# Kernel tuning notes

Measured on AMD Instinct MI355X. Metric: run time of the kernel, lower is better.

The kernel has to match this reference:

```python
import jax, jax.numpy as jnp
import numpy as np

E = 32      # particle_embed_dim = q/k/v head out dim
G = 2       # nof_net_types (conv groups)
NEG_SLOPE = 0.01


def _glin(x, w, b, groups):
    """Grouped 1x1 conv on (M, C, 1, 1) == grouped linear.
    x: (M, Cin), w: (Cout, Cin//groups), b: (Cout,)."""
    M = x.shape[0]
    Cout = w.shape[0]
    xg = x.reshape(M, groups, -1)                 # (M, G, Cin/G)
    wg = w.reshape(groups, Cout // groups, -1)    # (G, Cout/G, Cin/G)
    y = jnp.einsum('mgi,goi->mgo', xg, wg).reshape(M, Cout)
    return y + b


def setup_inputs() -> dict:
    key = jax.random.key(0)
    ks = jax.random.split(key, 9)
    B, N = 32, 1024
    s = 0.05
    return {
        'x_e':   jax.random.normal(ks[0], (B, N, G * E), dtype=jnp.float32),
        'w_qkv': jax.random.normal(ks[1], (3 * G * E, E), dtype=jnp.float32) * s,
        'b_qkv': jax.random.normal(ks[2], (3 * G * E,), dtype=jnp.float32) * s,
        'w_h1':  jax.random.normal(ks[3], (G * E, 2 * E), dtype=jnp.float32) * s,
        'b_h1':  jax.random.normal(ks[4], (G * E,), dtype=jnp.float32) * s,
        'w_h10': jax.random.normal(ks[5], (G * E, E), dtype=jnp.float32) * s,
        'b_h10': jax.random.normal(ks[6], (G * E,), dtype=jnp.float32) * s,
        'w_h11': jax.random.normal(ks[7], (G * E, E), dtype=jnp.float32) * s,
        'b_h11': jax.random.normal(ks[8], (G * E,), dtype=jnp.float32) * s,
    }


def reference(x_e, w_qkv, b_qkv, w_h1, b_h1, w_h10, b_h10, w_h11, b_h11):
    B, N, D = x_e.shape                      # D = G*E = 64
    act = lambda z: jnp.where(z >= 0, z, NEG_SLOPE * z)

    # grouped 1x1-conv QKV projection
    qkv = _glin(x_e.reshape(B * N, D), w_qkv, b_qkv, G)        # (B*N, 3*G*E)
    qkv = qkv.reshape(B, N, G, 3, E).transpose(0, 2, 3, 1, 4)  # (B, G, 3, N, E)
    q, k, v = qkv[:, :, 0], qkv[:, :, 1], qkv[:, :, 2]         # each (B, G, N, E)

    # NOTE: module divides k by sqrt(E) and logits by sqrt(E) again -> 1/E total
    scale = 1.0 / E
    ip = jnp.einsum('bgne,bgme->bgnm', q, k) * scale           # (B, G, N, N)
    sip = jax.nn.softmax(ip, axis=-1)
    attn = jnp.einsum('bgnm,bgme->bgne', sip, v)               # (B, G, N, E)

    # concat pre-attention v with attention output, regroup per-particle
    x_xe = jnp.concatenate([v, attn], axis=3)                  # (B, G, N, 2E)
    x_xe = x_xe.transpose(0, 2, 1, 3).reshape(B * N, G * 2 * E)  # (B*N, 128)

    h = act(_glin(x_xe, w_h1, b_h1, G))
    h = act(_glin(h, w_h10, b_h10, G))
    h = act(_glin(h, w_h11, b_h11, G))
    return h.reshape(B * N, G * E, 1, 1)
```

## Files before the change

kernel.cpp:

```cpp
#include <hip/hip_runtime.h>

#define B_ 32
#define N_ 1024
#define NEG 0.01f
#define QSC (1.4426950408889634f/32.0f)

using half8  = __attribute__((ext_vector_type(8))) _Float16;
using half4  = __attribute__((ext_vector_type(4))) _Float16;
using half2  = __attribute__((ext_vector_type(2))) _Float16;
using fp16x2 = __attribute__((ext_vector_type(2))) __fp16;
using floatx4 = __attribute__((ext_vector_type(4))) float;

#if defined(__has_builtin)
#if __has_builtin(__builtin_amdgcn_exp2f)
#define EXP2(x) __builtin_amdgcn_exp2f(x)
#endif
#endif
#ifndef EXP2
#define EXP2(x) exp2f(x)
#endif

__device__ inline half2 pkcvt(float a, float b) {
    fp16x2 r = __builtin_amdgcn_cvt_pkrtz(a, b);
    return __builtin_bit_cast(half2, r);
}

__device__ inline half8 cvt8(float4 a, float4 b) {
    half2 p0 = pkcvt(a.x, a.y);
    half2 p1 = pkcvt(a.z, a.w);
    half2 p2 = pkcvt(b.x, b.y);
    half2 p3 = pkcvt(b.z, b.w);
    half8 h = { p0[0],p0[1], p1[0],p1[1], p2[0],p2[1], p3[0],p3[1] };
    return h;
}

struct __align__(16) Smem {
    union {
        struct {
            _Float16 Kst[2][64*40];
            _Float16 Vtst[2][32*72];
            union {
                struct { _Float16 wsh[96*36]; float bsh[96]; } wg;
                _Float16 qs[64*40];
            } pq;
        } lp;
        _Float16 xs[64*72];
    } u;
    float linv[64];
    float bl1[32], bl10[32], bl11[32];
};

__global__ __launch_bounds__(256, 4) void fused_kernel(
    const float* __restrict__ x, const float* __restrict__ w_qkv, const float* __restrict__ b_qkv,
    const float* __restrict__ w_h1,  const float* __restrict__ b_h1,
    const float* __restrict__ w_h10, const float* __restrict__ b_h10,
    const float* __restrict__ w_h11, const float* __restrict__ b_h11,
    float* __restrict__ out)
{
    __shared__ Smem sm;
    int t = threadIdx.x;
    int bg = blockIdx.x >> 4;
    int qtile = blockIdx.x & 15;
    int b = bg >> 1, g = bg & 1;
    int qbase = qtile * 64;
    int lane = t & 63, w = t >> 6;
    int L15 = lane & 15, quad = lane >> 4;

    for (int idx = t; idx < 96*32; idx += 256) {
        int r = idx >> 5, c = idx & 31;
        float wv = w_qkv[(g*96 + r)*32 + c];
        sm.u.lp.pq.wg.wsh[r*36 + c] = (_Float16)(r < 32 ? wv*QSC : wv);
    }
    if (t < 96) sm.u.lp.pq.wg.bsh[t] = b_qkv[g*96 + t];
    if (t < 32) {
        sm.bl1[t]  = b_h1[g*32+t];
        sm.bl10[t] = b_h10[g*32+t];
        sm.bl11[t] = b_h11[g*32+t];
    }
    __syncthreads();

    half8 bwq[2], bwk[2], bwv[2];
    floatx4 cq[2], ck[2], cv[2];
    #pragma unroll
    for (int et = 0; et < 2; et++) {
        bwq[et] = *(const half8*)&sm.u.lp.pq.wg.wsh[(     et*16 + L15)*36 + quad*8];
        bwk[et] = *(const half8*)&sm.u.lp.pq.wg.wsh[(32 + et*16 + L15)*36 + quad*8];
        bwv[et] = *(const half8*)&sm.u.lp.pq.wg.wsh[(64 + et*16 + L15)*36 + quad*8];
        float bq = sm.u.lp.pq.wg.bsh[     et*16 + L15] * QSC;
        float bk = sm.u.lp.pq.wg.bsh[32 + et*16 + L15];
        float bv = sm.u.lp.pq.wg.bsh[64 + et*16 + L15];
        cq[et] = (floatx4){bq,bq,bq,bq};
        ck[et] = (floatx4){bk,bk,bk,bk};
        cv[et] = (floatx4){bv,bv,bv,bv};
    }
    __syncthreads();

    {
        const float* p = x + ((size_t)b*N_ + qbase + w*16 + L15)*64 + g*32 + quad*8;
        half8 axq = cvt8(*(const float4*)p, *(const float4*)(p + 4));
        floatx4 dq0 = __builtin_amdgcn_mfma_f32_16x16x32_f16(axq, bwq[0], cq[0], 0,0,0);
        floatx4 dq1 = __builtin_amdgcn_mfma_f32_16x16x32_f16(axq, bwq[1], cq[1], 0,0,0);
        #pragma unroll
        for (int r = 0; r < 4; r++) {
            sm.u.lp.pq.qs[(w*16 + quad*4 + r)*40 +      L15] = (_Float16)dq0[r];
            sm.u.lp.pq.qs[(w*16 + quad*4 + r)*40 + 16 + L15] = (_Float16)dq1[r];
        }
    }
    half8 bq = *(const half8*)&sm.u.lp.pq.qs[(w*16 + L15)*40 + quad*8];

    float4 xf0, xf1;
    auto prefetch = [&](int tile) {
        const float* p = x + ((size_t)b*N_ + tile*64 + w*16 + L15)*64 + g*32 + quad*8;
        xf0 = *(const float4*)p;
        xf1 = *(const float4*)(p + 4);
    };
    auto proj_tile = [&](int buf) {
        half8 axk = cvt8(xf0, xf1);
        floatx4 dK[2], dV[2];
        #pragma unroll
        for (int et = 0; et < 2; et++) {
            dK[et] = __builtin_amdgcn_mfma_f32_16x16x32_f16(axk, bwk[et], ck[et], 0,0,0);
            dV[et] = __builtin_amdgcn_mfma_f32_16x16x32_f16(axk, bwv[et], cv[et], 0,0,0);
        }
        int rb = w*16 + quad*4;
        #pragma unroll
        for (int et = 0; et < 2; et++) {
            half2 k01 = pkcvt(dK[et][0], dK[et][1]);
            half2 k23 = pkcvt(dK[et][2], dK[et][3]);
            half2 v01 = pkcvt(dV[et][0], dV[et][1]);
            half2 v23 = pkcvt(dV[et][2], dV[et][3]);
            half4 vh = { v01[0], v01[1], v23[0], v23[1] };
            sm.u.lp.Kst[buf][(rb+0)*40 + et*16 + L15] = k01[0];
            sm.u.lp.Kst[buf][(rb+1)*40 + et*16 + L15] = k01[1];
            sm.u.lp.Kst[buf][(rb+2)*40 + et*16 + L15] = k23[0];
            sm.u.lp.Kst[buf][(rb+3)*40 + et*16 + L15] = k23[1];
            *(half4*)&sm.u.lp.Vtst[buf][(et*16 + L15)*72 + rb] = vh;
        }
    };

    prefetch(0);
    proj_tile(0);
    __syncthreads();

    floatx4 o0 = {0.f,0.f,0.f,0.f}, o1 = o0;
    float lsum = 0.f;

    for (int kt = 0; kt < 16; kt++) {
        int cur = kt & 1;
        if (kt < 15) prefetch(kt + 1);
        #pragma unroll
        for (int mt8 = 0; mt8 < 4; mt8++) {
            half8 ak = *(const half8*)&sm.u.lp.Kst[cur][(mt8*16 + L15)*40 + quad*8];
            floatx4 zz = {0.f,0.f,0.f,0.f};
            floatx4 s = __builtin_amdgcn_mfma_f32_16x16x32_f16(ak, bq, zz, 0,0,0);
            float p0 = EXP2(s.x), p1 = EXP2(s.y), p2 = EXP2(s.z), p3 = EXP2(s.w);
            lsum += (p0+p1)+(p2+p3);
            half2 pa = pkcvt(p0, p1);
            half2 pb = pkcvt(p2, p3);
            half4 a0 = { pa[0], pa[1], pb[0], pb[1] };
            half4 bv0 = *(const half4*)&sm.u.lp.Vtst[cur][      L15*72 + mt8*16 + quad*4];
            half4 bv1 = *(const half4*)&sm.u.lp.Vtst[cur][(16 + L15)*72 + mt8*16 + quad*4];
            o0 = __builtin_amdgcn_mfma_f32_16x16x16f16(a0, bv0, o0, 0,0,0);
            o1 = __builtin_amdgcn_mfma_f32_16x16x16f16(a0, bv1, o1, 0,0,0);
        }
        if (kt < 15) proj_tile(1 - cur);
        __syncthreads();
    }

    lsum += __shfl_xor(lsum, 16, 64); lsum += __shfl_xor(lsum, 32, 64);
    if (quad == 0) sm.linv[w*16 + L15] = 1.0f / lsum;

    {
        const float* p = x + ((size_t)b*N_ + qbase + w*16 + L15)*64 + g*32 + quad*8;
        half8 axv = cvt8(*(const float4*)p, *(const float4*)(p + 4));
        floatx4 dv0 = __builtin_amdgcn_mfma_f32_16x16x32_f16(axv, bwv[0], cv[0], 0,0,0);
        floatx4 dv1 = __builtin_amdgcn_mfma_f32_16x16x32_f16(axv, bwv[1], cv[1], 0,0,0);
        #pragma unroll
        for (int r = 0; r < 4; r++) {
            sm.u.xs[(w*16 + quad*4 + r)*72 +      L15] = (_Float16)dv0[r];
            sm.u.xs[(w*16 + quad*4 + r)*72 + 16 + L15] = (_Float16)dv1[r];
        }
    }
    {
        float4 li = *(const float4*)&sm.linv[w*16 + quad*4];
        const floatx4* ofr[2] = { &o0, &o1 };
        #pragma unroll
        for (int et = 0; et < 2; et++) {
            floatx4 ov = *ofr[et];
            sm.u.xs[(w*16+quad*4+0)*72 + 32 + et*16 + L15] = (_Float16)(ov[0]*li.x);
            sm.u.xs[(w*16+quad*4+1)*72 + 32 + et*16 + L15] = (_Float16)(ov[1]*li.y);
            sm.u.xs[(w*16+quad*4+2)*72 + 32 + et*16 + L15] = (_Float16)(ov[2]*li.z);
            sm.u.xs[(w*16+quad*4+3)*72 + 32 + et*16 + L15] = (_Float16)(ov[3]*li.w);
        }
    }

    half4 a1f[2][4], a2f[2][2], a3f[2][2];
    #pragma unroll
    for (int mt = 0; mt < 2; mt++) {
        #pragma unroll
        for (int kt = 0; kt < 4; kt++) {
            float4 f = *(const float4*)(w_h1 + (size_t)(g*32+mt*16+L15)*64 + kt*16 + quad*4);
            half2 ha = pkcvt(f.x, f.y);
            half2 hb = pkcvt(f.z, f.w);
            half4 h = { ha[0], ha[1], hb[0], hb[1] };
            a1f[mt][kt] = h;
        }
        #pragma unroll
        for (int kt = 0; kt < 2; kt++) {
            float4 f = *(const float4*)(w_h10 + (size_t)(g*32+mt*16+L15)*32 + kt*16 + quad*4);
            half2 ha = pkcvt(f.x, f.y);
            half2 hb = pkcvt(f.z, f.w);
            half4 h = { ha[0], ha[1], hb[0], hb[1] };
            a2f[mt][kt] = h;
            float4 f2 = *(const float4*)(w_h11 + (size_t)(g*32+mt*16+L15)*32 + kt*16 + quad*4);
            half2 hc = pkcvt(f2.x, f2.y);
            half2 hd = pkcvt(f2.z, f2.w);
            half4 h2 = { hc[0], hc[1], hd[0], hd[1] };
            a3f[mt][kt] = h2;
        }
    }

    floatx4 d1[2];
    #pragma unroll
    for (int mt = 0; mt < 2; mt++) {
        float4 bb = *(const float4*)&sm.bl1[mt*16 + quad*4];
        d1[mt] = (floatx4){ bb.x, bb.y, bb.z, bb.w };
    }
    #pragma unroll
    for (int kt = 0; kt < 4; kt++) {
        half4 b1 = *(const half4*)&sm.u.xs[(w*16+L15)*72 + kt*16 + quad*4];
        d1[0] = __builtin_amdgcn_mfma_f32_16x16x16f16(a1f[0][kt], b1, d1[0], 0,0,0);
        d1[1] = __builtin_amdgcn_mfma_f32_16x16x16f16(a1f[1][kt], b1, d1[1], 0,0,0);
    }
    half4 h1b[2];
    #pragma unroll
    for (int mt = 0; mt < 2; mt++) {
        float v0 = d1[mt][0]; v0 = (v0>=0.f)?v0:NEG*v0;
        float v1 = d1[mt][1]; v1 = (v1>=0.f)?v1:NEG*v1;
        float v2 = d1[mt][2]; v2 = (v2>=0.f)?v2:NEG*v2;
        float v3 = d1[mt][3]; v3 = (v3>=0.f)?v3:NEG*v3;
        half2 ha = pkcvt(v0, v1);
        half2 hb = pkcvt(v2, v3);
        half4 h = { ha[0], ha[1], hb[0], hb[1] };
        h1b[mt] = h;
    }
    floatx4 d2[2];
    #pragma unroll
    for (int mt = 0; mt < 2; mt++) {
        float4 bb = *(const float4*)&sm.bl10[mt*16 + quad*4];
        d2[mt] = (floatx4){ bb.x, bb.y, bb.z, bb.w };
    }
    #pragma unroll
    for (int mt = 0; mt < 2; mt++)
        #pragma unroll
        for (int kt = 0; kt < 2; kt++)
            d2[mt] = __builtin_amdgcn_mfma_f32_16x16x16f16(a2f[mt][kt], h1b[kt], d2[mt], 0,0,0);
    half4 h2b[2];
    #pragma unroll
    for (int mt = 0; mt < 2; mt++) {
        float v0 = d2[mt][0]; v0 = (v0>=0.f)?v0:NEG*v0;
        float v1 = d2[mt][1]; v1 = (v1>=0.f)?v1:NEG*v1;
        float v2 = d2[mt][2]; v2 = (v2>=0.f)?v2:NEG*v2;
        float v3 = d2[mt][3]; v3 = (v3>=0.f)?v3:NEG*v3;
        half2 ha = pkcvt(v0, v1);
        half2 hb = pkcvt(v2, v3);
        half4 h = { ha[0], ha[1], hb[0], hb[1] };
        h2b[mt] = h;
    }
    floatx4 d3[2];
    #pragma unroll
    for (int mt = 0; mt < 2; mt++) {
        float4 bb = *(const float4*)&sm.bl11[mt*16 + quad*4];
        d3[mt] = (floatx4){ bb.x, bb.y, bb.z, bb.w };
    }
    #pragma unroll
    for (int mt = 0; mt < 2; mt++)
        #pragma unroll
        for (int kt = 0; kt < 2; kt++)
            d3[mt] = __builtin_amdgcn_mfma_f32_16x16x16f16(a3f[mt][kt], h2b[kt], d3[mt], 0,0,0);
    #pragma unroll
    for (int mt = 0; mt < 2; mt++) {
        float4 ov;
        ov.x = d3[mt][0]; ov.x = (ov.x>=0.f)?ov.x:NEG*ov.x;
        ov.y = d3[mt][1]; ov.y = (ov.y>=0.f)?ov.y:NEG*ov.y;
        ov.z = d3[mt][2]; ov.z = (ov.z>=0.f)?ov.z:NEG*ov.z;
        ov.w = d3[mt][3]; ov.w = (ov.w>=0.f)?ov.w:NEG*ov.w;
        *(float4*)(out + ((size_t)b*N_ + qbase + w*16 + L15)*64 + g*32 + mt*16 + quad*4) = ov;
    }
}

extern "C" void kernel_launch(void* const* d_in, const int* in_sizes, int n_in,
                              void* d_out, int out_size, void* d_ws, size_t ws_size,
                              hipStream_t stream) {
    const float* x_e   = (const float*)d_in[0];
    const float* w_qkv = (const float*)d_in[1];
    const float* b_qkv = (const float*)d_in[2];
    const float* w_h1  = (const float*)d_in[3];
    const float* b_h1  = (const float*)d_in[4];
    const float* w_h10 = (const float*)d_in[5];
    const float* b_h10 = (const float*)d_in[6];
    const float* w_h11 = (const float*)d_in[7];
    const float* b_h11 = (const float*)d_in[8];
    float* out = (float*)d_out;

    hipLaunchKernelGGL(fused_kernel, dim3(B_*2*16), dim3(256), 0, stream,
                       x_e, w_qkv, b_qkv, w_h1, b_h1, w_h10, b_h10, w_h11, b_h11, out);
}
```

Before: 107.9 us.

## Double query and key tile size to 128 with 512-thread blocks

After: 105.9 us. About the same (-1.8%).

```diff
diff --git a/kernel.cpp b/kernel.cpp
--- a/kernel.cpp
+++ b/kernel.cpp
@@ -35,22 +35,18 @@
 }
 
 struct __align__(16) Smem {
+    _Float16 Kst[2][128*40];
+    _Float16 Vtst[2][32*132];
     union {
-        struct {
-            _Float16 Kst[2][64*40];
-            _Float16 Vtst[2][32*72];
-            union {
-                struct { _Float16 wsh[96*36]; float bsh[96]; } wg;
-                _Float16 qs[64*40];
-            } pq;
-        } lp;
-        _Float16 xs[64*72];
+        struct { _Float16 wsh[96*36]; float bsh[96]; } wg;
+        _Float16 qs[128*40];
+        _Float16 xs[128*72];
     } u;
-    float linv[64];
+    float linv[128];
     float bl1[32], bl10[32], bl11[32];
 };
 
-__global__ __launch_bounds__(256, 4) void fused_kernel(
+__global__ __launch_bounds__(512, 4) void fused_kernel(
     const float* __restrict__ x, const float* __restrict__ w_qkv, const float* __restrict__ b_qkv,
     const float* __restrict__ w_h1,  const float* __restrict__ b_h1,
     const float* __restrict__ w_h10, const float* __restrict__ b_h10,
@@ -59,19 +55,19 @@
 {
     __shared__ Smem sm;
     int t = threadIdx.x;
-    int bg = blockIdx.x >> 4;
-    int qtile = blockIdx.x & 15;
+    int bg = blockIdx.x >> 3;
+    int qtile = blockIdx.x & 7;
     int b = bg >> 1, g = bg & 1;
-    int qbase = qtile * 64;
+    int qbase = qtile * 128;
     int lane = t & 63, w = t >> 6;
     int L15 = lane & 15, quad = lane >> 4;
 
-    for (int idx = t; idx < 96*32; idx += 256) {
+    for (int idx = t; idx < 96*32; idx += 512) {
         int r = idx >> 5, c = idx & 31;
         float wv = w_qkv[(g*96 + r)*32 + c];
-        sm.u.lp.pq.wg.wsh[r*36 + c] = (_Float16)(r < 32 ? wv*QSC : wv);
-    }
-    if (t < 96) sm.u.lp.pq.wg.bsh[t] = b_qkv[g*96 + t];
+        sm.u.wg.wsh[r*36 + c] = (_Float16)(r < 32 ? wv*QSC : wv);
+    }
+    if (t < 96) sm.u.wg.bsh[t] = b_qkv[g*96 + t];
     if (t < 32) {
         sm.bl1[t]  = b_h1[g*32+t];
         sm.bl10[t] = b_h10[g*32+t];
@@ -83,12 +79,12 @@
     floatx4 cq[2], ck[2], cv[2];
     #pragma unroll
     for (int et = 0; et < 2; et++) {
-        bwq[et] = *(const half8*)&sm.u.lp.pq.wg.wsh[(     et*16 + L15)*36 + quad*8];
-        bwk[et] = *(const half8*)&sm.u.lp.pq.wg.wsh[(32 + et*16 + L15)*36 + quad*8];
-        bwv[et] = *(const half8*)&sm.u.lp.pq.wg.wsh[(64 + et*16 + L15)*36 + quad*8];
-        float bq = sm.u.lp.pq.wg.bsh[     et*16 + L15] * QSC;
-        float bk = sm.u.lp.pq.wg.bsh[32 + et*16 + L15];
-        float bv = sm.u.lp.pq.wg.bsh[64 + et*16 + L15];
+        bwq[et] = *(const half8*)&sm.u.wg.wsh[(     et*16 + L15)*36 + quad*8];
+        bwk[et] = *(const half8*)&sm.u.wg.wsh[(32 + et*16 + L15)*36 + quad*8];
+        bwv[et] = *(const half8*)&sm.u.wg.wsh[(64 + et*16 + L15)*36 + quad*8];
+        float bq = sm.u.wg.bsh[     et*16 + L15] * QSC;
+        float bk = sm.u.wg.bsh[32 + et*16 + L15];
+        float bv = sm.u.wg.bsh[64 + et*16 + L15];
         cq[et] = (floatx4){bq,bq,bq,bq};
         ck[et] = (floatx4){bk,bk,bk,bk};
         cv[et] = (floatx4){bv,bv,bv,bv};
@@ -102,15 +98,15 @@
         floatx4 dq1 = __builtin_amdgcn_mfma_f32_16x16x32_f16(axq, bwq[1], cq[1], 0,0,0);
         #pragma unroll
         for (int r = 0; r < 4; r++) {
-            sm.u.lp.pq.qs[(w*16 + quad*4 + r)*40 +      L15] = (_Float16)dq0[r];
-            sm.u.lp.pq.qs[(w*16 + quad*4 + r)*40 + 16 + L15] = (_Float16)dq1[r];
-        }
-    }
-    half8 bq = *(const half8*)&sm.u.lp.pq.qs[(w*16 + L15)*40 + quad*8];
+            sm.u.qs[(w*16 + quad*4 + r)*40 +      L15] = (_Float16)dq0[r];
+            sm.u.qs[(w*16 + quad*4 + r)*40 + 16 + L15] = (_Float16)dq1[r];
+        }
+    }
+    half8 bq = *(const half8*)&sm.u.qs[(w*16 + L15)*40 + quad*8];
 
     float4 xf0, xf1;
     auto prefetch = [&](int tile) {
-        const float* p = x + ((size_t)b*N_ + tile*64 + w*16 + L15)*64 + g*32 + quad*8;
+        const float* p = x + ((size_t)b*N_ + tile*128 + w*16 + L15)*64 + g*32 + quad*8;
         xf0 = *(const float4*)p;
         xf1 = *(const float4*)(p + 4);
     };
@@ -130,11 +126,11 @@
             half2 v01 = pkcvt(dV[et][0], dV[et][1]);
             half2 v23 = pkcvt(dV[et][2], dV[et][3]);
             half4 vh = { v01[0], v01[1], v23[0], v23[1] };
-            sm.u.lp.Kst[buf][(rb+0)*40 + et*16 + L15] = k01[0];
-            sm.u.lp.Kst[buf][(rb+1)*40 + et*16 + L15] = k01[1];
-            sm.u.lp.Kst[buf][(rb+2)*40 + et*16 + L15] = k23[0];
-            sm.u.lp.Kst[buf][(rb+3)*40 + et*16 + L15] = k23[1];
-            *(half4*)&sm.u.lp.Vtst[buf][(et*16 + L15)*72 + rb] = vh;
+            sm.Kst[buf][(rb+0)*40 + et*16 + L15] = k01[0];
+            sm.Kst[buf][(rb+1)*40 + et*16 + L15] = k01[1];
+            sm.Kst[buf][(rb+2)*40 + et*16 + L15] = k23[0];
+            sm.Kst[buf][(rb+3)*40 + et*16 + L15] = k23[1];
+            *(half4*)&sm.Vtst[buf][(et*16 + L15)*132 + rb] = vh;
         }
     };
 
@@ -145,12 +141,12 @@
     floatx4 o0 = {0.f,0.f,0.f,0.f}, o1 = o0;
     float lsum = 0.f;
 
-    for (int kt = 0; kt < 16; kt++) {
+    for (int kt = 0; kt < 8; kt++) {
         int cur = kt & 1;
-        if (kt < 15) prefetch(kt + 1);
-        #pragma unroll
-        for (int mt8 = 0; mt8 < 4; mt8++) {
-            half8 ak = *(const half8*)&sm.u.lp.Kst[cur][(mt8*16 + L15)*40 + quad*8];
+        if (kt < 7) prefetch(kt + 1);
+        #pragma unroll
+        for (int m8 = 0; m8 < 8; m8++) {
+            half8 ak = *(const half8*)&sm.Kst[cur][(m8*16 + L15)*40 + quad*8];
             floatx4 zz = {0.f,0.f,0.f,0.f};
             floatx4 s = __builtin_amdgcn_mfma_f32_16x16x32_f16(ak, bq, zz, 0,0,0);
             float p0 = EXP2(s.x), p1 = EXP2(s.y), p2 = EXP2(s.z), p3 = EXP2(s.w);
@@ -158,12 +154,12 @@
             half2 pa = pkcvt(p0, p1);
             half2 pb = pkcvt(p2, p3);
             half4 a0 = { pa[0], pa[1], pb[0], pb[1] };
-            half4 bv0 = *(const half4*)&sm.u.lp.Vtst[cur][      L15*72 + mt8*16 + quad*4];
-            half4 bv1 = *(const half4*)&sm.u.lp.Vtst[cur][(16 + L15)*72 + mt8*16 + quad*4];
+            half4 bv0 = *(const half4*)&sm.Vtst[cur][      L15*132 + m8*16 + quad*4];
+            half4 bv1 = *(const half4*)&sm.Vtst[cur][(16 + L15)*132 + m8*16 + quad*4];
             o0 = __builtin_amdgcn_mfma_f32_16x16x16f16(a0, bv0, o0, 0,0,0);
             o1 = __builtin_amdgcn_mfma_f32_16x16x16f16(a0, bv1, o1, 0,0,0);
         }
-        if (kt < 15) proj_tile(1 - cur);
+        if (kt < 7) proj_tile(1 - cur);
         __syncthreads();
     }
 
@@ -303,6 +299,6 @@
     const float* b_h11 = (const float*)d_in[8];
     float* out = (float*)d_out;
 
-    hipLaunchKernelGGL(fused_kernel, dim3(B_*2*16), dim3(256), 0, stream,
+    hipLaunchKernelGGL(fused_kernel, dim3(B_*2*8), dim3(512), 0, stream,
                        x_e, w_qkv, b_qkv, w_h1, b_h1, w_h10, b_h10, w_h11, b_h11, out);
 }
```
